# Kernel optimization log

Measured on AMD Instinct MI355X. Metric: run time of the kernel, lower is better.

Reference implementation:

```python
import jax, jax.numpy as jnp
import numpy as np

N = 131072  # nodes processed in one frontier/level batch
H = 256     # h_size
X = 256     # x_size


def setup_inputs() -> dict:
    key = jax.random.key(0)
    ks = jax.random.split(key, 8)
    def w(k, shape, fan_in):
        return jax.random.normal(k, shape, jnp.float32) / np.float32(np.sqrt(fan_in))
    return {
        "x": jax.random.normal(ks[0], (N, X), jnp.float32),
        "child_h": jax.random.normal(ks[1], (N, H), jnp.float32),
        "child_c": jax.random.normal(ks[2], (N, H), jnp.float32),
        "child_idx": jax.random.randint(ks[3], (N,), 0, N, jnp.int32),
        "W_iou_w": w(ks[4], (3 * H, X), X),
        "U_iou_w": w(ks[5], (3 * H, H), H),
        "b_iou": jnp.zeros((1, 3 * H), jnp.float32),
        "W_f_w": w(ks[6], (H, X), X),
        "W_f_b": jnp.zeros((H,), jnp.float32),
        "U_f_w": w(ks[7], (H, H), H),
        "U_f_b": jnp.zeros((H,), jnp.float32),
        "b_f": jnp.zeros((1, H), jnp.float32),
    }


def reference(x, child_h, child_c, child_idx, W_iou_w, U_iou_w, b_iou,
              W_f_w, W_f_b, U_f_w, U_f_b, b_f):
    # Node-local projections (precomputed 'Wx' / 'Wfx' node data in the DGL module)
    Wx = x @ W_iou_w.T                      # [N, 3H]
    Wfx = x @ W_f_w.T + W_f_b               # [N, H] (nn.Linear bias included)
    # message_func + mailbox gather (one child per node; see shape analysis)
    hc = child_h[child_idx]                 # [N, H] irregular gather
    cc = child_c[child_idx]                 # [N, H]
    # reduce_func: forget gate + masked sum over children (K=1)
    f = jax.nn.sigmoid(Wfx + hc @ U_f_w.T + U_f_b + b_f)  # [N, H]
    c_red = f * cc                          # sum over 1 child
    iou = Wx + b_iou + hc @ U_iou_w.T       # [N, 3H]
    # apply_node_func: gated combine
    i, o, u = jnp.split(iou, 3, axis=1)
    c = jax.nn.sigmoid(i) * jnp.tanh(u) + c_red
    h = jax.nn.sigmoid(o) * jnp.tanh(c)
    return h, c
```

## Files before the change

kernel.cpp:

```cpp
#include <hip/hip_runtime.h>


typedef unsigned short u16;
typedef unsigned int u32;
typedef __bf16 bf16x8 __attribute__((ext_vector_type(8)));
typedef float f32x16 __attribute__((ext_vector_type(16)));
typedef u16 u16x4 __attribute__((ext_vector_type(4)));
typedef u16 u16x8 __attribute__((ext_vector_type(8)));

#define NTOT 131072
#define NHOFF ((size_t)131072 * 256)
#define AS1 __attribute__((address_space(1)))
#define AS3 __attribute__((address_space(3)))

__device__ __forceinline__ u16 f2bf(float f) {
  u32 u = __float_as_uint(f);
  return (u16)((u + 0x7FFFu + ((u >> 16) & 1u)) >> 16);
}

__global__ void prep_w_frag(const float* __restrict__ Wiou, const float* __restrict__ Uiou,
                            const float* __restrict__ Wf, const float* __restrict__ Uf,
                            u16* __restrict__ BpackF) {
  int c = blockIdx.x * 256 + threadIdx.x;
  int np = c & 255;
  int r = c >> 8;
  int hi = r & 1; r >>= 1;
  int ks = r & 3; r >>= 2;
  int kt = r & 7; r >>= 3;
  int g  = r & 3;
  int j = (np >> 6) * 256 + g * 64 + (np & 63);
  int k0 = kt * 64 + ks * 16 + hi * 8;
  const float* src;
  if (j < 768) src = (k0 < 256) ? (Wiou + (size_t)j * 256 + k0) : (Uiou + (size_t)j * 256 + (k0 - 256));
  else { int jj = j - 768; src = (k0 < 256) ? (Wf + (size_t)jj * 256 + k0) : (Uf + (size_t)jj * 256 + (k0 - 256)); }
  float4 f0 = *(const float4*)(src);
  float4 f1 = *(const float4*)(src + 4);
  u16x8 v;
  v[0] = f2bf(f0.x); v[1] = f2bf(f0.y); v[2] = f2bf(f0.z); v[3] = f2bf(f0.w);
  v[4] = f2bf(f1.x); v[5] = f2bf(f1.y); v[6] = f2bf(f1.z); v[7] = f2bf(f1.w);
  *(u16x8*)(BpackF + (size_t)c * 8) = v;
}

__global__ void prep_w_legacy(const float* __restrict__ Wiou, const float* __restrict__ Uiou,
                              const float* __restrict__ Wf, const float* __restrict__ Uf,
                              u16* __restrict__ Bpack) {
  int cid = blockIdx.x * 256 + threadIdx.x;
  int j = cid >> 6;
  int kc = cid & 63;
  int k = kc * 8;
  int kt = kc >> 3, k8 = kc & 7;
  int s = j >> 8, g = (j >> 6) & 3, e = j & 63;
  int c = s * 64 + e;
  const float* src;
  if (j < 768) src = (k < 256) ? (Wiou + j * 256 + k) : (Uiou + j * 256 + (k - 256));
  else { int jj = j - 768; src = (k < 256) ? (Wf + jj * 256 + k) : (Uf + jj * 256 + (k - 256)); }
  float4 f0 = *(const float4*)(src);
  float4 f1 = *(const float4*)(src + 4);
  u16x8 v;
  v[0] = f2bf(f0.x); v[1] = f2bf(f0.y); v[2] = f2bf(f0.z); v[3] = f2bf(f0.w);
  v[4] = f2bf(f1.x); v[5] = f2bf(f1.y); v[6] = f2bf(f1.z); v[7] = f2bf(f1.w);
  int slot = (g * 8 + kt) * 2048 + ((c * 8 + k8) ^ (c & 7));
  *(u16x8*)(Bpack + slot * 8) = v;
}

__global__ void prep_bias(const float* __restrict__ biou, const float* __restrict__ wfb,
                          const float* __restrict__ ufb, const float* __restrict__ bfv,
                          float* __restrict__ Bias) {
  int j = blockIdx.x * 256 + threadIdx.x;
  Bias[j] = (j < 768) ? biou[j] : (wfb[j - 768] + ufb[j - 768] + bfv[j - 768]);
}

__global__ void prep_apack(const float* __restrict__ x, const float* __restrict__ ch,
                           const int* __restrict__ cidx, u16* __restrict__ Apack) {
  int e = blockIdx.x * 256 + threadIdx.x;
  int n = e >> 6, c = e & 63;
  const float* src = (c < 32) ? (x + (size_t)n * 256 + c * 8)
                              : (ch + (size_t)cidx[n] * 256 + (c - 32) * 8);
  float4 f0 = *(const float4*)src;
  float4 f1 = *(const float4*)(src + 4);
  u16x8 v;
  v[0] = f2bf(f0.x); v[1] = f2bf(f0.y); v[2] = f2bf(f0.z); v[3] = f2bf(f0.w);
  v[4] = f2bf(f1.x); v[5] = f2bf(f1.y); v[6] = f2bf(f1.z); v[7] = f2bf(f1.w);
  *(u16x8*)(Apack + (size_t)n * 512 + c * 8) = v;
}

__global__ __launch_bounds__(256, 3)
void treelstm_main_v8(const u16* __restrict__ Apack, const u16* __restrict__ BpackF,
                      const float* __restrict__ Bias, const float* __restrict__ child_c,
                      const int* __restrict__ cidx, float* __restrict__ out) {
  __shared__ __align__(16) u16 ldsA[2 * 4096];
  __shared__ int lds_cidx[64];
  char* ldsByte = (char*)ldsA;

  const int tid = threadIdx.x;
  const int orig = blockIdx.x;
  const int bid = (orig & 7) * 1024 + (orig >> 3);
  const int g = bid & 3;
  const int n0 = (bid >> 2) * 64;

  if (tid < 64) lds_cidx[tid] = cidx[n0 + tid];

  const int lane = tid & 63, w = tid >> 6;
  const int wm = w >> 1, wn = w & 1;
  const int lr = lane & 31, hi = lane >> 5;

  const u16* aSrc = Apack + (size_t)(n0 + (tid >> 3)) * 512
                    + (((tid & 7) ^ ((tid >> 3) & 7)) << 3);
  const u16* bP = BpackF + (size_t)g * 131072 + (size_t)hi * 2048 + (size_t)(wn * 32 + lr) * 8;

  const int arowB = (wm * 32 + lr) * 128;
  int aoff[4];
  #pragma unroll
  for (int ks = 0; ks < 4; ++ks) aoff[ks] = (ks * 32 + hi * 16) ^ ((lr & 7) << 4);

  f32x16 acc[4] = {};

  #define STAGE_A(T)                                                            \
    { _Pragma("unroll") for (int q = 0; q < 2; ++q)                             \
        __builtin_amdgcn_global_load_lds(                                       \
            (const AS1 void*)(aSrc + (T) * 64 + q * 16384),                     \
            (AS3 void*)(ldsByte + ((T) & 1) * 8192 + q * 4096 + w * 1024),      \
            16, 0, 0); }

  STAGE_A(0);

  #pragma unroll
  for (int t = 0; t < 8; ++t) {
    bf16x8 b01[4][2];
    #pragma unroll
    for (int nf = 0; nf < 4; ++nf)
      #pragma unroll
      for (int kk = 0; kk < 2; ++kk)
        b01[nf][kk] = *(const bf16x8*)(bP + (size_t)t * 16384 + kk * 4096 + nf * 512);
    __builtin_amdgcn_sched_barrier(0);
    asm volatile("s_waitcnt vmcnt(8) lgkmcnt(0)\n\ts_barrier" ::: "memory");
    __builtin_amdgcn_sched_barrier(0);
    const char* bufA = ldsByte + (t & 1) * 8192;
    bf16x8 af[4];
    #pragma unroll
    for (int ks = 0; ks < 4; ++ks)
      af[ks] = *(const bf16x8*)(bufA + arowB + aoff[ks]);
    __builtin_amdgcn_s_setprio(1);
    #pragma unroll
    for (int kk = 0; kk < 2; ++kk)
      #pragma unroll
      for (int nf = 0; nf < 4; ++nf)
        acc[nf] = __builtin_amdgcn_mfma_f32_32x32x16_bf16(af[kk], b01[nf][kk],
                                                          acc[nf], 0, 0, 0);
    __builtin_amdgcn_s_setprio(0);
    bf16x8 b23[4][2];
    #pragma unroll
    for (int nf = 0; nf < 4; ++nf)
      #pragma unroll
      for (int kk = 0; kk < 2; ++kk)
        b23[nf][kk] = *(const bf16x8*)(bP + (size_t)t * 16384 + (kk + 2) * 4096 + nf * 512);
    if (t < 7) STAGE_A(t + 1);
    __builtin_amdgcn_s_setprio(1);
    #pragma unroll
    for (int kk = 0; kk < 2; ++kk)
      #pragma unroll
      for (int nf = 0; nf < 4; ++nf)
        acc[nf] = __builtin_amdgcn_mfma_f32_32x32x16_bf16(af[kk + 2], b23[nf][kk],
                                                          acc[nf], 0, 0, 0);
    __builtin_amdgcn_s_setprio(0);
  }
  #undef STAGE_A

  const int hcol = g * 64 + wn * 32 + lr;
  float b4[4];
  #pragma unroll
  for (int nf = 0; nf < 4; ++nf) b4[nf] = Bias[nf * 256 + hcol];
  #pragma unroll
  for (int reg = 0; reg < 16; ++reg) {
    int rowb = wm * 32 + (reg & 3) + 8 * (reg >> 2) + 4 * hi;
    size_t n = (size_t)(n0 + rowb);
    float i_ = acc[0][reg] + b4[0];
    float o_ = acc[1][reg] + b4[1];
    float u_ = acc[2][reg] + b4[2];
    float fp = acc[3][reg] + b4[3];
    float ccv = child_c[(size_t)lds_cidx[rowb] * 256 + hcol];
    float sigi = 1.f / (1.f + __expf(-i_));
    float sigo = 1.f / (1.f + __expf(-o_));
    float sigf = 1.f / (1.f + __expf(-fp));
    float tu = 2.f / (1.f + __expf(-2.f * u_)) - 1.f;
    float c = sigi * tu + sigf * ccv;
    float tc = 2.f / (1.f + __expf(-2.f * c)) - 1.f;
    out[n * 256 + hcol] = sigo * tc;
    out[NHOFF + n * 256 + hcol] = c;
  }
}

__global__ __launch_bounds__(256, 2)
void treelstm_main_f32(const float* __restrict__ x, const float* __restrict__ child_h,
                       const float* __restrict__ child_c, const int* __restrict__ cidx,
                       const u16* __restrict__ Bpack, const float* __restrict__ Bias,
                       float* __restrict__ out) {
  __shared__ __align__(16) u16 ldsA[128 * 64];
  __shared__ __align__(16) u16 ldsB[256 * 64];
  __shared__ int lds_cidx[128];

  const int tid = threadIdx.x;
  const int n0 = blockIdx.x * 128;
  const int g = blockIdx.y;

  if (tid < 128) lds_cidx[tid] = cidx[n0 + tid];

  const int lane = tid & 63, w = tid >> 6;
  const int wm = w >> 1, wn = w & 1;
  const int lr = lane & 31, hi = lane >> 5;

  f32x16 acc[2][4] = {};

  const char* ldsAb = (const char*)ldsA;
  const char* ldsBb = (const char*)ldsB;
  int arow[2];
  #pragma unroll
  for (int mi = 0; mi < 2; mi++) arow[mi] = (wm * 64 + mi * 32 + lr) * 128;
  const int aswz = (lr & 7) << 4;
  int brow[4];
  #pragma unroll
  for (int s = 0; s < 4; s++) brow[s] = (s * 64 + wn * 32 + lr) * 128;
  const int bswz = (lr & 7) << 4;

  for (int kt = 0; kt < 8; ++kt) {
    #pragma unroll
    for (int q = 0; q < 8; ++q) {
      int v = q * 256 + tid;
      int r = v >> 4;
      int kq = (v & 15) * 4;
      const float* src = (kt < 4) ? (x + (size_t)(n0 + r) * 256 + kt * 64 + kq)
                                  : (child_h + (size_t)lds_cidx[r] * 256 + (kt - 4) * 64 + kq);
      float4 d = *(const float4*)src;
      u16x4 b;
      b[0] = f2bf(d.x); b[1] = f2bf(d.y); b[2] = f2bf(d.z); b[3] = f2bf(d.w);
      int addr = (r * 128 + kq * 2) ^ ((r & 7) << 4);
      *(u16x4*)((char*)ldsA + addr) = b;
    }
    const u16* bsrc = Bpack + (g * 8 + kt) * 16384;
    #pragma unroll
    for (int q = 0; q < 8; ++q) {
      int m = q * 256 + tid;
      *(u16x8*)((char*)ldsB + m * 16) = *(const u16x8*)(bsrc + m * 8);
    }
    __syncthreads();
    #pragma unroll
    for (int ks = 0; ks < 4; ++ks) {
      int kb = ks * 32 + hi * 16;
      bf16x8 af[2], bfr[4];
      #pragma unroll
      for (int mi = 0; mi < 2; mi++)
        af[mi] = *(const bf16x8*)(ldsAb + ((arow[mi] + kb) ^ aswz));
      #pragma unroll
      for (int s = 0; s < 4; s++)
        bfr[s] = *(const bf16x8*)(ldsBb + ((brow[s] + kb) ^ bswz));
      #pragma unroll
      for (int mi = 0; mi < 2; mi++)
        #pragma unroll
        for (int s = 0; s < 4; s++)
          acc[mi][s] = __builtin_amdgcn_mfma_f32_32x32x16_bf16(af[mi], bfr[s], acc[mi][s], 0, 0, 0);
    }
    __syncthreads();
  }

  const int tcol = g * 64 + wn * 32 + lr;
  const float bi = Bias[tcol], bo = Bias[256 + tcol], bu = Bias[512 + tcol], bfg = Bias[768 + tcol];
  #pragma unroll
  for (int mi = 0; mi < 2; mi++) {
    #pragma unroll
    for (int reg = 0; reg < 16; ++reg) {
      int row = wm * 64 + mi * 32 + (reg & 3) + 8 * (reg >> 2) + 4 * hi;
      int n = n0 + row;
      float i_ = acc[mi][0][reg] + bi;
      float o_ = acc[mi][1][reg] + bo;
      float u_ = acc[mi][2][reg] + bu;
      float fp = acc[mi][3][reg] + bfg;
      float ccv = child_c[(size_t)lds_cidx[row] * 256 + tcol];
      float sigi = 1.f / (1.f + __expf(-i_));
      float sigo = 1.f / (1.f + __expf(-o_));
      float sigf = 1.f / (1.f + __expf(-fp));
      float tu = 2.f / (1.f + __expf(-2.f * u_)) - 1.f;
      float c = sigi * tu + sigf * ccv;
      float tc = 2.f / (1.f + __expf(-2.f * c)) - 1.f;
      out[(size_t)n * 256 + tcol] = sigo * tc;
      out[NHOFF + (size_t)n * 256 + tcol] = c;
    }
  }
}

extern "C" void kernel_launch(void* const* d_in, const int* in_sizes, int n_in,
                              void* d_out, int out_size, void* d_ws, size_t ws_size,
                              hipStream_t stream) {
  const float* x    = (const float*)d_in[0];
  const float* ch   = (const float*)d_in[1];
  const float* cc   = (const float*)d_in[2];
  const int*   ci   = (const int*)d_in[3];
  const float* Wiou = (const float*)d_in[4];
  const float* Uiou = (const float*)d_in[5];
  const float* biou = (const float*)d_in[6];
  const float* Wf   = (const float*)d_in[7];
  const float* Wfb  = (const float*)d_in[8];
  const float* Uf   = (const float*)d_in[9];
  const float* Ufb  = (const float*)d_in[10];
  const float* bfv  = (const float*)d_in[11];

  u16* Bpack = (u16*)d_ws;
  float* Bias = (float*)((char*)d_ws + (1 << 20));
  u16* Apack = (u16*)((char*)d_ws + (2 << 20));

  const size_t need = (size_t)(2 << 20) + (size_t)NTOT * 512 * sizeof(u16);

  prep_bias<<<4, 256, 0, stream>>>(biou, Wfb, Ufb, bfv, Bias);

  if (ws_size >= need) {
    prep_w_frag<<<256, 256, 0, stream>>>(Wiou, Uiou, Wf, Uf, Bpack);
    prep_apack<<<32768, 256, 0, stream>>>(x, ch, ci, Apack);
    treelstm_main_v8<<<8192, 256, 0, stream>>>(Apack, Bpack, Bias, cc, ci, (float*)d_out);
  } else {
    prep_w_legacy<<<256, 256, 0, stream>>>(Wiou, Uiou, Wf, Uf, Bpack);
    dim3 grid(1024, 4);
    treelstm_main_f32<<<grid, 256, 0, stream>>>(x, ch, cc, ci, Bpack, Bias, (float*)d_out);
  }
}
```

Measured before the change: 352.1 us.

## Give each wave a private LDS A buffer and drop block barriers in GEMM loop

Each wave now stages its own 32-row A slice into a private double-buffered LDS region, so the per-iteration s_barrier is removed and only vmcnt waits are used. The prefetch of the next A tile is issued earlier, before the wait, and the block-to-tile mapping changes so that the gate group is the slowest-varying index. The two waves sharing wm now each load the same A rows, which doubles A traffic into LDS and doubles LDS use. Occupancy hint drops from 3 to 2 blocks per CU.

New measurement: 396.1 us. +12.5%, slower.

```diff
diff --git a/kernel.cpp b/kernel.cpp
--- a/kernel.cpp
+++ b/kernel.cpp
@@ -84,45 +84,47 @@
   *(u16x8*)(Apack + (size_t)n * 512 + c * 8) = v;
 }
 
-__global__ __launch_bounds__(256, 3)
-void treelstm_main_v8(const u16* __restrict__ Apack, const u16* __restrict__ BpackF,
-                      const float* __restrict__ Bias, const float* __restrict__ child_c,
-                      const int* __restrict__ cidx, float* __restrict__ out) {
-  __shared__ __align__(16) u16 ldsA[2 * 4096];
+__global__ __launch_bounds__(256, 2)
+void treelstm_v11(const u16* __restrict__ Apack, const u16* __restrict__ BpackF,
+                  const float* __restrict__ Bias, const float* __restrict__ child_c,
+                  const int* __restrict__ cidx, float* __restrict__ out) {
+  __shared__ __align__(16) char ldsA[4 * 8192];
   __shared__ int lds_cidx[64];
-  char* ldsByte = (char*)ldsA;
 
   const int tid = threadIdx.x;
   const int orig = blockIdx.x;
-  const int bid = (orig & 7) * 1024 + (orig >> 3);
-  const int g = bid & 3;
-  const int n0 = (bid >> 2) * 64;
+  const int g = orig >> 11;
+  const int rt = orig & 2047;
+  const int rt2 = (rt & 7) * 256 + (rt >> 3);
+  const int n0 = rt2 * 64;
 
   if (tid < 64) lds_cidx[tid] = cidx[n0 + tid];
-
-  const int lane = tid & 63, w = tid >> 6;
+  __syncthreads();
+
+  const int l = tid & 63, w = tid >> 6;
   const int wm = w >> 1, wn = w & 1;
-  const int lr = lane & 31, hi = lane >> 5;
-
-  const u16* aSrc = Apack + (size_t)(n0 + (tid >> 3)) * 512
-                    + (((tid & 7) ^ ((tid >> 3) & 7)) << 3);
+  const int lr = l & 31, hi = l >> 5;
+
+  char* myBuf = ldsA + w * 8192;
+
+  const char* aSrc = (const char*)Apack + (size_t)(n0 + wm * 32 + (l >> 3)) * 1024
+                     + (((l & 7) ^ ((l >> 3) & 7)) << 4);
   const u16* bP = BpackF + (size_t)g * 131072 + (size_t)hi * 2048 + (size_t)(wn * 32 + lr) * 8;
 
-  const int arowB = (wm * 32 + lr) * 128;
-  int aoff[4];
-  #pragma unroll
-  for (int ks = 0; ks < 4; ++ks) aoff[ks] = (ks * 32 + hi * 16) ^ ((lr & 7) << 4);
+  const int arow = lr * 128;
+  int koff[4];
+  #pragma unroll
+  for (int ks = 0; ks < 4; ++ks) koff[ks] = (ks * 32 + hi * 16) ^ ((lr & 7) << 4);
 
   f32x16 acc[4] = {};
 
-  #define STAGE_A(T)                                                            \
-    { _Pragma("unroll") for (int q = 0; q < 2; ++q)                             \
+  #define ST(T)                                                                 \
+    { _Pragma("unroll") for (int q = 0; q < 4; ++q)                             \
         __builtin_amdgcn_global_load_lds(                                       \
-            (const AS1 void*)(aSrc + (T) * 64 + q * 16384),                     \
-            (AS3 void*)(ldsByte + ((T) & 1) * 8192 + q * 4096 + w * 1024),      \
-            16, 0, 0); }
-
-  STAGE_A(0);
+            (const AS1 void*)(aSrc + (T) * 128 + q * 8192),                     \
+            (AS3 void*)(myBuf + ((T) & 1) * 4096 + q * 1024), 16, 0, 0); }
+
+  ST(0);
 
   #pragma unroll
   for (int t = 0; t < 8; ++t) {
@@ -132,14 +134,16 @@
       #pragma unroll
       for (int kk = 0; kk < 2; ++kk)
         b01[nf][kk] = *(const bf16x8*)(bP + (size_t)t * 16384 + kk * 4096 + nf * 512);
+    if (t < 7) ST(t + 1);
     __builtin_amdgcn_sched_barrier(0);
-    asm volatile("s_waitcnt vmcnt(8) lgkmcnt(0)\n\ts_barrier" ::: "memory");
+    if (t < 7) asm volatile("s_waitcnt vmcnt(12)" ::: "memory");
+    else       asm volatile("s_waitcnt vmcnt(8)" ::: "memory");
     __builtin_amdgcn_sched_barrier(0);
-    const char* bufA = ldsByte + (t & 1) * 8192;
+    const char* buf = myBuf + (t & 1) * 4096;
     bf16x8 af[4];
     #pragma unroll
     for (int ks = 0; ks < 4; ++ks)
-      af[ks] = *(const bf16x8*)(bufA + arowB + aoff[ks]);
+      af[ks] = *(const bf16x8*)(buf + arow + koff[ks]);
     __builtin_amdgcn_s_setprio(1);
     #pragma unroll
     for (int kk = 0; kk < 2; ++kk)
@@ -154,7 +158,6 @@
       #pragma unroll
       for (int kk = 0; kk < 2; ++kk)
         b23[nf][kk] = *(const bf16x8*)(bP + (size_t)t * 16384 + (kk + 2) * 4096 + nf * 512);
-    if (t < 7) STAGE_A(t + 1);
     __builtin_amdgcn_s_setprio(1);
     #pragma unroll
     for (int kk = 0; kk < 2; ++kk)
@@ -164,7 +167,7 @@
                                                           acc[nf], 0, 0, 0);
     __builtin_amdgcn_s_setprio(0);
   }
-  #undef STAGE_A
+  #undef ST
 
   const int hcol = g * 64 + wn * 32 + lr;
   float b4[4];
@@ -314,7 +317,7 @@
   if (ws_size >= need) {
     prep_w_frag<<<256, 256, 0, stream>>>(Wiou, Uiou, Wf, Uf, Bpack);
     prep_apack<<<32768, 256, 0, stream>>>(x, ch, ci, Apack);
-    treelstm_main_v8<<<8192, 256, 0, stream>>>(Apack, Bpack, Bias, cc, ci, (float*)d_out);
+    treelstm_v11<<<8192, 256, 0, stream>>>(Apack, Bpack, Bias, cc, ci, (float*)d_out);
   } else {
     prep_w_legacy<<<256, 256, 0, stream>>>(Wiou, Uiou, Wf, Uf, Bpack);
     dim3 grid(1024, 4);
```
